# Kernel optimization log

Hardware: AMD Instinct MI355X
Metric: run time of the kernel (lower is better)

## Reference

```python
import jax, jax.numpy as jnp
import numpy as np

B, T, D = 256, 512, 256

def setup_inputs() -> dict:
    key = jax.random.key(0)
    k1, k2, k3, k4 = jax.random.split(key, 4)
    ip = jax.random.normal(k1, (B, T, D), dtype=jnp.float32)
    W = jax.random.normal(k2, (D, D), dtype=jnp.float32) * (1.0 / np.sqrt(D))
    b = jax.random.normal(k3, (D,), dtype=jnp.float32) * 0.05
    context = jax.random.normal(k4, (D, 1), dtype=jnp.float32) * 0.05
    return {"ip": ip, "W": W, "b": b, "context": context}

def reference(ip, W, b, context) -> jnp.ndarray:
    # linear -> tanh: [B, T, D]
    h = jnp.tanh(jnp.einsum("btd,ed->bte", ip, W) + b)
    # attention scores over words: [B, T]
    scores = jnp.einsum("btd,d->bt", h, context[:, 0])
    attn = jax.nn.softmax(scores, axis=1)
    # weighted sum over words -> sentence embeddings: [B, D]
    sent_embeds = jnp.einsum("bt,btd->bd", attn, ip)
    return sent_embeds
```

## Files before the change

### kernel.cpp

```cpp
#include <hip/hip_runtime.h>
#include <hip/hip_bf16.h>

#define NBATCH 256
#define NT 512
#define ND 256
#define NROWS (NBATCH * NT)

typedef __attribute__((ext_vector_type(8))) short short8;
typedef __attribute__((ext_vector_type(4))) float floatx4;

__device__ __forceinline__ unsigned short f2bf(float x) {
    unsigned int u = __float_as_uint(x);
    u += 0x7FFFu + ((u >> 16) & 1u);
    return (unsigned short)(u >> 16);
}

__global__ void __launch_bounds__(256) prep_kernel(
    const float* __restrict__ W, unsigned short* __restrict__ wf)
{
    int g  = blockIdx.x * 256 + threadIdx.x;
    int m  = g & 15, q = (g >> 4) & 3, s = (g >> 6) & 7, nb = g >> 9;
    const float* src = W + (nb * 16 + m) * ND + q * 8 + s * 32;
    float4 f0 = *(const float4*)src;
    float4 f1 = *(const float4*)(src + 4);
    short8 v;
    v[0] = (short)f2bf(f0.x); v[1] = (short)f2bf(f0.y);
    v[2] = (short)f2bf(f0.z); v[3] = (short)f2bf(f0.w);
    v[4] = (short)f2bf(f1.x); v[5] = (short)f2bf(f1.y);
    v[6] = (short)f2bf(f1.z); v[7] = (short)f2bf(f1.w);
    *(short8*)(wf + (long)g * 8) = v;
}

__global__ void __launch_bounds__(256, 3) scores_kernel(
    const float* __restrict__ ip,
    const unsigned short* __restrict__ wf,
    const float* __restrict__ bias,
    const float* __restrict__ ctx,
    float* __restrict__ scores)
{
    __shared__ __align__(16) char wsm[32768];
    __shared__ float bias_s[ND];
    __shared__ float ctx_s[ND];

    const int tid  = threadIdx.x;
    const int lane = tid & 63;
    const int wv   = tid >> 6;
    const int m    = lane & 15;
    const int q    = lane >> 4;
    const long row0 = (long)blockIdx.x * 128 + wv * 32;

    bias_s[tid] = bias[tid];
    ctx_s[tid]  = ctx[tid];

    short8 a[2][8];
#pragma unroll
    for (int tile = 0; tile < 2; ++tile) {
        const float* ar = ip + (row0 + tile * 16 + m) * ND + q * 8;
#pragma unroll
        for (int s = 0; s < 8; ++s) {
            float4 f0 = *(const float4*)(ar + s * 32);
            float4 f1 = *(const float4*)(ar + s * 32 + 4);
            short8 v;
            v[0] = (short)f2bf(f0.x); v[1] = (short)f2bf(f0.y);
            v[2] = (short)f2bf(f0.z); v[3] = (short)f2bf(f0.w);
            v[4] = (short)f2bf(f1.x); v[5] = (short)f2bf(f1.y);
            v[6] = (short)f2bf(f1.z); v[7] = (short)f2bf(f1.w);
            a[tile][s] = v;
        }
    }

    float sc0[4] = {0.f, 0.f, 0.f, 0.f};
    float sc1[4] = {0.f, 0.f, 0.f, 0.f};
    const short8* wchunks = (const short8*)wf;
    short8* wsm16 = (short8*)wsm;

#pragma unroll 1
    for (int stage = 0; stage < 4; ++stage) {
        if (stage) __syncthreads();
#pragma unroll
        for (int u = 0; u < 8; ++u) {
            int c = u * 256 + tid;
            wsm16[c] = wchunks[stage * 2048 + c];
        }
        __syncthreads();

#pragma unroll 1
        for (int nbl = 0; nbl < 4; ++nbl) {
            const int e = (stage * 4 + nbl) * 16 + m;
            const short8* wp = wsm16 + nbl * 512 + lane;
            short8 w[8];
#pragma unroll
            for (int s = 0; s < 8; ++s) w[s] = wp[s * 64];
            floatx4 acc0 = {0.f, 0.f, 0.f, 0.f};
            floatx4 acc1 = {0.f, 0.f, 0.f, 0.f};
#pragma unroll
            for (int s = 0; s < 8; ++s) {
                acc0 = __builtin_amdgcn_mfma_f32_16x16x32_bf16(a[0][s], w[s], acc0, 0, 0, 0);
                acc1 = __builtin_amdgcn_mfma_f32_16x16x32_bf16(a[1][s], w[s], acc1, 0, 0, 0);
            }
            const float be  = bias_s[e];
            const float ce  = ctx_s[e];
            const float ce2 = ce + ce;
#pragma unroll
            for (int r = 0; r < 4; ++r) {
                float x0 = acc0[r] + be;
                float x1 = acc1[r] + be;
                float t0 = __builtin_amdgcn_rcpf(__expf(x0 + x0) + 1.f);
                float t1 = __builtin_amdgcn_rcpf(__expf(x1 + x1) + 1.f);
                sc0[r] = __builtin_fmaf(-ce2, t0, sc0[r] + ce);
                sc1[r] = __builtin_fmaf(-ce2, t1, sc1[r] + ce);
            }
        }
    }

#pragma unroll
    for (int off = 8; off >= 1; off >>= 1) {
#pragma unroll
        for (int r = 0; r < 4; ++r) {
            sc0[r] += __shfl_xor(sc0[r], off, 64);
            sc1[r] += __shfl_xor(sc1[r], off, 64);
        }
    }
    if (m == 0) {
#pragma unroll
        for (int r = 0; r < 4; ++r) {
            scores[row0 + q * 4 + r]      = sc0[r];
            scores[row0 + 16 + q * 4 + r] = sc1[r];
        }
    }
}

__global__ void __launch_bounds__(256) wsum_kernel(
    const float* __restrict__ ip,
    const float* __restrict__ scores,
    float* __restrict__ out)
{
    __shared__ float attn_s[NT];
    __shared__ float red[8];
    __shared__ float partial[16][64];

    const int b  = blockIdx.x >> 2;
    const int dq = blockIdx.x & 3;
    const int tid  = threadIdx.x;
    const int lane = tid & 63;
    const int wv   = tid >> 6;

    float s0 = scores[(long)b * NT + tid];
    float s1 = scores[(long)b * NT + tid + 256];
    float mx = fmaxf(s0, s1);
#pragma unroll
    for (int off = 32; off >= 1; off >>= 1) mx = fmaxf(mx, __shfl_xor(mx, off, 64));
    if (lane == 0) red[wv] = mx;
    __syncthreads();
    mx = fmaxf(fmaxf(red[0], red[1]), fmaxf(red[2], red[3]));
    float e0 = __expf(s0 - mx), e1 = __expf(s1 - mx);
    float sm = e0 + e1;
#pragma unroll
    for (int off = 32; off >= 1; off >>= 1) sm += __shfl_xor(sm, off, 64);
    __syncthreads();
    if (lane == 0) red[4 + wv] = sm;
    __syncthreads();
    sm = red[4] + red[5] + red[6] + red[7];
    float inv = 1.f / sm;
    attn_s[tid]       = e0 * inv;
    attn_s[tid + 256] = e1 * inv;
    __syncthreads();

    const int dg = tid & 15;
    const int ts = tid >> 4;
    const float4* base = (const float4*)(ip + (long)b * NT * ND + dq * 64) + dg;
    float a0 = 0.f, a1 = 0.f, a2 = 0.f, a3 = 0.f;
#pragma unroll 8
    for (int t = ts * 32; t < ts * 32 + 32; ++t) {
        float w = attn_s[t];
        float4 v = base[t * 64];
        a0 += w * v.x; a1 += w * v.y; a2 += w * v.z; a3 += w * v.w;
    }
    partial[ts][dg * 4 + 0] = a0;
    partial[ts][dg * 4 + 1] = a1;
    partial[ts][dg * 4 + 2] = a2;
    partial[ts][dg * 4 + 3] = a3;
    __syncthreads();
    if (tid < 64) {
        float r = 0.f;
#pragma unroll
        for (int i = 0; i < 16; ++i) r += partial[i][tid];
        out[(long)b * ND + dq * 64 + tid] = r;
    }
}

extern "C" void kernel_launch(void* const* d_in, const int* in_sizes, int n_in,
                              void* d_out, int out_size, void* d_ws, size_t ws_size,
                              hipStream_t stream) {
    const float* ip   = (const float*)d_in[0];
    const float* W    = (const float*)d_in[1];
    const float* bias = (const float*)d_in[2];
    const float* ctx  = (const float*)d_in[3];

    unsigned short* wf = (unsigned short*)d_ws;
    float* scores = (float*)((char*)d_ws + ND * ND * sizeof(unsigned short));

    prep_kernel<<<32, 256, 0, stream>>>(W, wf);
    scores_kernel<<<NROWS / 128, 256, 0, stream>>>(ip, wf, bias, ctx, scores);
    wsum_kernel<<<NBATCH * 4, 256, 0, stream>>>(ip, scores, (float*)d_out);
}
```

Baseline: 233.3 us.

## Halve rows per wave in scores kernel to raise occupancy

Each wave of the scores kernel now handles one 16-row tile instead of two, which halves the register-held A fragments and doubles the grid size. The launch bound rises from 3 to 4 blocks per SM. Bias and context are read from global memory instead of being staged in shared memory. The input loads are grouped so more float4 loads are in flight before conversion. In exchange, the W tile reuse per LDS load is halved, so each block reads W from global and LDS twice as often per row.

```diff
diff --git a/kernel.cpp b/kernel.cpp
--- a/kernel.cpp
+++ b/kernel.cpp
@@ -31,7 +31,7 @@
     *(short8*)(wf + (long)g * 8) = v;
 }
 
-__global__ void __launch_bounds__(256, 3) scores_kernel(
+__global__ void __launch_bounds__(256, 4) scores_kernel(
     const float* __restrict__ ip,
     const unsigned short* __restrict__ wf,
     const float* __restrict__ bias,
@@ -39,40 +39,40 @@
     float* __restrict__ scores)
 {
     __shared__ __align__(16) char wsm[32768];
-    __shared__ float bias_s[ND];
-    __shared__ float ctx_s[ND];
+    short8* lds16 = (short8*)wsm;
 
     const int tid  = threadIdx.x;
     const int lane = tid & 63;
     const int wv   = tid >> 6;
     const int m    = lane & 15;
     const int q    = lane >> 4;
-    const long row0 = (long)blockIdx.x * 128 + wv * 32;
+    const long row0 = (long)blockIdx.x * 64 + wv * 16;
 
-    bias_s[tid] = bias[tid];
-    ctx_s[tid]  = ctx[tid];
-
-    short8 a[2][8];
+    short8 a[8];
+    {
+        const float* ar = ip + (row0 + m) * ND + q * 8;
+        float4 raw[8];
 #pragma unroll
-    for (int tile = 0; tile < 2; ++tile) {
-        const float* ar = ip + (row0 + tile * 16 + m) * ND + q * 8;
+        for (int g = 0; g < 2; ++g) {
 #pragma unroll
-        for (int s = 0; s < 8; ++s) {
-            float4 f0 = *(const float4*)(ar + s * 32);
-            float4 f1 = *(const float4*)(ar + s * 32 + 4);
-            short8 v;
-            v[0] = (short)f2bf(f0.x); v[1] = (short)f2bf(f0.y);
-            v[2] = (short)f2bf(f0.z); v[3] = (short)f2bf(f0.w);
-            v[4] = (short)f2bf(f1.x); v[5] = (short)f2bf(f1.y);
-            v[6] = (short)f2bf(f1.z); v[7] = (short)f2bf(f1.w);
-            a[tile][s] = v;
+            for (int i = 0; i < 4; ++i) {
+                raw[2 * i]     = *(const float4*)(ar + (4 * g + i) * 32);
+                raw[2 * i + 1] = *(const float4*)(ar + (4 * g + i) * 32 + 4);
+            }
+#pragma unroll
+            for (int i = 0; i < 4; ++i) {
+                short8 v;
+                v[0] = (short)f2bf(raw[2 * i].x); v[1] = (short)f2bf(raw[2 * i].y);
+                v[2] = (short)f2bf(raw[2 * i].z); v[3] = (short)f2bf(raw[2 * i].w);
+                v[4] = (short)f2bf(raw[2 * i + 1].x); v[5] = (short)f2bf(raw[2 * i + 1].y);
+                v[6] = (short)f2bf(raw[2 * i + 1].z); v[7] = (short)f2bf(raw[2 * i + 1].w);
+                a[4 * g + i] = v;
+            }
         }
     }
 
-    float sc0[4] = {0.f, 0.f, 0.f, 0.f};
-    float sc1[4] = {0.f, 0.f, 0.f, 0.f};
+    float sc[4] = {0.f, 0.f, 0.f, 0.f};
     const short8* wchunks = (const short8*)wf;
-    short8* wsm16 = (short8*)wsm;
 
 #pragma unroll 1
     for (int stage = 0; stage < 4; ++stage) {
@@ -80,35 +80,29 @@
 #pragma unroll
         for (int u = 0; u < 8; ++u) {
             int c = u * 256 + tid;
-            wsm16[c] = wchunks[stage * 2048 + c];
+            lds16[c] = wchunks[stage * 2048 + c];
         }
         __syncthreads();
 
 #pragma unroll 1
         for (int nbl = 0; nbl < 4; ++nbl) {
             const int e = (stage * 4 + nbl) * 16 + m;
-            const short8* wp = wsm16 + nbl * 512 + lane;
+            const short8* wp = lds16 + nbl * 512 + lane;
             short8 w[8];
 #pragma unroll
             for (int s = 0; s < 8; ++s) w[s] = wp[s * 64];
-            floatx4 acc0 = {0.f, 0.f, 0.f, 0.f};
-            floatx4 acc1 = {0.f, 0.f, 0.f, 0.f};
+            floatx4 acc = {0.f, 0.f, 0.f, 0.f};
 #pragma unroll
-            for (int s = 0; s < 8; ++s) {
-                acc0 = __builtin_amdgcn_mfma_f32_16x16x32_bf16(a[0][s], w[s], acc0, 0, 0, 0);
-                acc1 = __builtin_amdgcn_mfma_f32_16x16x32_bf16(a[1][s], w[s], acc1, 0, 0, 0);
-            }
-            const float be  = bias_s[e];
-            const float ce  = ctx_s[e];
+            for (int s = 0; s < 8; ++s)
+                acc = __builtin_amdgcn_mfma_f32_16x16x32_bf16(a[s], w[s], acc, 0, 0, 0);
+            const float be  = bias[e];
+            const float ce  = ctx[e];
             const float ce2 = ce + ce;
 #pragma unroll
             for (int r = 0; r < 4; ++r) {
-                float x0 = acc0[r] + be;
-                float x1 = acc1[r] + be;
-                float t0 = __builtin_amdgcn_rcpf(__expf(x0 + x0) + 1.f);
-                float t1 = __builtin_amdgcn_rcpf(__expf(x1 + x1) + 1.f);
-                sc0[r] = __builtin_fmaf(-ce2, t0, sc0[r] + ce);
-                sc1[r] = __builtin_fmaf(-ce2, t1, sc1[r] + ce);
+                float x = acc[r] + be;
+                float t = __builtin_amdgcn_rcpf(__expf(x + x) + 1.f);
+                sc[r] = __builtin_fmaf(-ce2, t, sc[r] + ce);
             }
         }
     }
@@ -116,17 +110,13 @@
 #pragma unroll
     for (int off = 8; off >= 1; off >>= 1) {
 #pragma unroll
-        for (int r = 0; r < 4; ++r) {
-            sc0[r] += __shfl_xor(sc0[r], off, 64);
-            sc1[r] += __shfl_xor(sc1[r], off, 64);
-        }
+        for (int r = 0; r < 4; ++r)
+            sc[r] += __shfl_xor(sc[r], off, 64);
     }
     if (m == 0) {
 #pragma unroll
-        for (int r = 0; r < 4; ++r) {
-            scores[row0 + q * 4 + r]      = sc0[r];
-            scores[row0 + 16 + q * 4 + r] = sc1[r];
-        }
+        for (int r = 0; r < 4; ++r)
+            scores[row0 + q * 4 + r] = sc[r];
     }
 }
 
@@ -201,6 +191,6 @@
     float* scores = (float*)((char*)d_ws + ND * ND * sizeof(unsigned short));
 
     prep_kernel<<<32, 256, 0, stream>>>(W, wf);
-    scores_kernel<<<NROWS / 128, 256, 0, stream>>>(ip, wf, bias, ctx, scores);
+    scores_kernel<<<NROWS / 64, 256, 0, stream>>>(ip, wf, bias, ctx, scores);
     wsum_kernel<<<NBATCH * 4, 256, 0, stream>>>(ip, scores, (float*)d_out);
 }
```

Measured after the change: 232.6 us. About the same (-0.3%).
